# Optimization experiments

Measured on AMD Instinct MI355X. Metric: run time of the kernel, lower is better.

Reference implementation:

```python
import jax, jax.numpy as jnp
import numpy as np

N = 50000      # nodes
E = 500000     # edges
D_IN = 64      # node_in_dim
K = 4          # edge_in_dim
H = 64         # node_hidden_dim
C = 40         # num_class
L = 2          # num_layers


def setup_inputs() -> dict:
    key = jax.random.key(0)
    ks = jax.random.split(key, 10)
    node_features = jax.random.normal(ks[0], (N, D_IN), jnp.float32)
    edge_features = jax.random.normal(ks[1], (L, E, K), jnp.float32)
    src = jax.random.randint(ks[2], (E,), 0, N)
    dst = jax.random.randint(ks[3], (E,), 0, N)
    W0 = jax.random.normal(ks[4], (K * D_IN, H), jnp.float32) * 0.05
    b0 = jnp.zeros((H,), jnp.float32)
    W1 = jax.random.normal(ks[5], (K * H, H), jnp.float32) * 0.05
    b1 = jnp.zeros((H,), jnp.float32)
    Wfc = jax.random.normal(ks[6], (H, C), jnp.float32) * 0.05
    bfc = jnp.zeros((C,), jnp.float32)
    return dict(node_features=node_features, edge_features=edge_features,
                src=src, dst=dst, W0=W0, b0=b0, W1=W1, b1=b1, Wfc=Wfc, bfc=bfc)


def reference(node_features, edge_features, src, dst, W0, b0, W1, b1, Wfc, bfc):
    h = node_features  # [N, d]
    ones = jnp.ones((E,), jnp.float32)
    cnt = jnp.maximum(jax.ops.segment_sum(ones, dst, num_segments=N), 1.0)  # in-degree
    for i, (W, b) in enumerate([(W0, b0), (W1, b1)]):
        e = edge_features[i]          # [E, K]
        hs = h[src]                   # [E, d] edge gather of src node features
        d = hs.shape[1]
        # message: relu(Linear(flatten(e[:,:,None] * h[:,None,:])))
        # flatten order is (K, d), so reshape W -> [K, d, H] and contract directly
        Wr = W.reshape(K, d, H)
        m = jax.nn.relu(jnp.einsum('ek,ed,kdh->eh', e, hs, Wr) + b)  # [E, H]
        s = jax.ops.segment_sum(m, dst, num_segments=N)              # scatter-sum
        h = jax.nn.relu(s / cnt[:, None])                            # mailbox mean + relu
    return h @ Wfc + bfc  # [N, C]
```

## Files before the change

### kernel.cpp

```cpp
#include <hip/hip_runtime.h>
#include <hip/hip_fp16.h>

#define N_NODES 50000
#define N_EDGES 500000
#define DIM 64
#define KDIM 4
#define HID 64
#define NCLS 40
#define NBLK ((N_NODES + 255) / 256)

__device__ inline unsigned pack2(float a, float b) {
    __half2 h = __floats2half2_rn(a, b);
    return *(unsigned*)&h;
}
__device__ inline float2 unpack2(unsigned u) {
    __half2 h = *(__half2*)&u;
    return __half22float2(h);
}

__global__ void hist_k(const int* __restrict__ dst, int* __restrict__ cnt) {
    int e = blockIdx.x * 256 + threadIdx.x;
    if (e < N_EDGES) atomicAdd(&cnt[dst[e]], 1);
}

__global__ __launch_bounds__(256) void scan_k(const int* __restrict__ cnt,
                                              int* __restrict__ start,
                                              int* __restrict__ cursor,
                                              volatile int* __restrict__ bflag,
                                              volatile int* __restrict__ bval) {
    __shared__ int ls[256];
    __shared__ int sbase;
    __shared__ int ok_all;
    int b = blockIdx.x, t = threadIdx.x;
    int n = b * 256 + t;
    int v = (n < N_NODES) ? cnt[n] : 0;
    ls[t] = v;
    __syncthreads();
#pragma unroll
    for (int off = 1; off < 256; off <<= 1) {
        int u = (t >= off) ? ls[t - off] : 0;
        __syncthreads();
        ls[t] += u;
        __syncthreads();
    }
    int incl = ls[t];
    int total = ls[255];
    __syncthreads();

    if (t == 0) {
        bval[b] = total;
        __threadfence();
        bflag[b] = 1;
    }

    if (b > 0) {
        for (;;) {
            int f = (t < b) ? bflag[t] : 1;
            if (t == 0) ok_all = 1;
            __syncthreads();
            if (!f) ok_all = 0;
            __syncthreads();
            if (ok_all) break;
        }
        __threadfence();
        int pv = (t < b) ? bval[t] : 0;
        ls[t] = pv;
        __syncthreads();
#pragma unroll
        for (int off = 128; off > 0; off >>= 1) {
            if (t < off) ls[t] += ls[t + off];
            __syncthreads();
        }
        if (t == 0) sbase = ls[0];
        __syncthreads();
    } else {
        if (t == 0) sbase = 0;
        __syncthreads();
    }

    int excl = sbase + incl - v;
    if (n < N_NODES) { start[n] = excl; cursor[n] = excl; }
    if (n == 0) start[N_NODES] = N_EDGES;
}

__global__ void scatter_k(const int* __restrict__ src, const int* __restrict__ dst,
                          const float* __restrict__ ef, int* __restrict__ cursor,
                          uint4* __restrict__ rec) {
    int e = blockIdx.x * 256 + threadIdx.x;
    if (e < N_EDGES) {
        int d = dst[e];
        int pos = atomicAdd(&cursor[d], 1);
        int sn = src[e];
        float4 f0 = ((const float4*)ef)[e];
        float4 f1 = ((const float4*)ef)[N_EDGES + e];
        rec[2 * pos]     = make_uint4((unsigned)sn, pack2(f0.x, f0.y), pack2(f0.z, f0.w), 0u);
        rec[2 * pos + 1] = make_uint4((unsigned)sn, pack2(f1.x, f1.y), pack2(f1.z, f1.w), 0u);
    }
}

__global__ __launch_bounds__(256) void transform_k(const float* __restrict__ hin,
                                                   const float* __restrict__ W,
                                                   unsigned* __restrict__ y) {
    __shared__ float sW[2 * 64 * 64];
    __shared__ float sh[64 * 65];
    int t = threadIdx.x;
    int kpair = blockIdx.y;

    const float4* W4 = (const float4*)(W + (size_t)kpair * 2 * 4096);
    float4* sW4 = (float4*)sW;
#pragma unroll
    for (int i = 0; i < 8; ++i) sW4[t + 256 * i] = W4[t + 256 * i];

    int n0 = blockIdx.x * 64;
#pragma unroll
    for (int i = 0; i < 4; ++i) {
        int idx = t + 256 * i;
        int nl = idx >> 4;
        int dg = idx & 15;
        int n = n0 + nl;
        float4 v = make_float4(0.f, 0.f, 0.f, 0.f);
        if (n < N_NODES) v = ((const float4*)hin)[(size_t)n * 16 + dg];
        sh[nl * 65 + dg * 4 + 0] = v.x;
        sh[nl * 65 + dg * 4 + 1] = v.y;
        sh[nl * 65 + dg * 4 + 2] = v.z;
        sh[nl * 65 + dg * 4 + 3] = v.w;
    }
    __syncthreads();

    int nl = t & 31;
    int cg = t >> 5;
    int k_local = cg >> 2;
    int hc0 = (cg & 3) * 16;

    float acc0[16], acc1[16];
#pragma unroll
    for (int j = 0; j < 16; ++j) { acc0[j] = 0.f; acc1[j] = 0.f; }

    for (int d = 0; d < 64; ++d) {
        float a0 = sh[nl * 65 + d];
        float a1 = sh[(nl + 32) * 65 + d];
        const float* wr = &sW[k_local * 4096 + d * 64 + hc0];
#pragma unroll
        for (int j = 0; j < 16; ++j) {
            float w = wr[j];
            acc0[j] = fmaf(a0, w, acc0[j]);
            acc1[j] = fmaf(a1, w, acc1[j]);
        }
    }

    int n_a = n0 + nl, n_b = n0 + nl + 32;
    int cbase = (kpair * 2 + k_local) * 64 + hc0;
    if (n_a < N_NODES) {
        uint4* o = (uint4*)(y + ((size_t)n_a * 256 + cbase) / 2);
        o[0] = make_uint4(pack2(acc0[0], acc0[1]), pack2(acc0[2], acc0[3]),
                          pack2(acc0[4], acc0[5]), pack2(acc0[6], acc0[7]));
        o[1] = make_uint4(pack2(acc0[8], acc0[9]), pack2(acc0[10], acc0[11]),
                          pack2(acc0[12], acc0[13]), pack2(acc0[14], acc0[15]));
    }
    if (n_b < N_NODES) {
        uint4* o = (uint4*)(y + ((size_t)n_b * 256 + cbase) / 2);
        o[0] = make_uint4(pack2(acc1[0], acc1[1]), pack2(acc1[2], acc1[3]),
                          pack2(acc1[4], acc1[5]), pack2(acc1[6], acc1[7]));
        o[1] = make_uint4(pack2(acc1[8], acc1[9]), pack2(acc1[10], acc1[11]),
                          pack2(acc1[12], acc1[13]), pack2(acc1[14], acc1[15]));
    }
}

__device__ inline void load_edge(const uint4 r, const unsigned* __restrict__ y,
                                 int lane, uint2& q0, uint2& q1, uint2& q2, uint2& q3) {
    int sn = (int)r.x;
    const uint2* yb = (const uint2*)(y + (size_t)sn * 128);
    q0 = yb[lane];
    q1 = yb[16 + lane];
    q2 = yb[32 + lane];
    q3 = yb[48 + lane];
}

__device__ inline void compute_edge(const uint4 r, uint2 q0, uint2 q1, uint2 q2, uint2 q3,
                                    const float4 bias, float4& acc) {
    float2 e01 = unpack2(r.y);
    float2 e23 = unpack2(r.z);
    float2 a0 = unpack2(q0.x), a1 = unpack2(q0.y);
    float2 b0 = unpack2(q1.x), b1 = unpack2(q1.y);
    float2 c0 = unpack2(q2.x), c1 = unpack2(q2.y);
    float2 d0 = unpack2(q3.x), d1 = unpack2(q3.y);

    float4 z = bias;
    z.x = fmaf(e01.x, a0.x, z.x); z.y = fmaf(e01.x, a0.y, z.y);
    z.z = fmaf(e01.x, a1.x, z.z); z.w = fmaf(e01.x, a1.y, z.w);
    z.x = fmaf(e01.y, b0.x, z.x); z.y = fmaf(e01.y, b0.y, z.y);
    z.z = fmaf(e01.y, b1.x, z.z); z.w = fmaf(e01.y, b1.y, z.w);
    z.x = fmaf(e23.x, c0.x, z.x); z.y = fmaf(e23.x, c0.y, z.y);
    z.z = fmaf(e23.x, c1.x, z.z); z.w = fmaf(e23.x, c1.y, z.w);
    z.x = fmaf(e23.y, d0.x, z.x); z.y = fmaf(e23.y, d0.y, z.y);
    z.z = fmaf(e23.y, d1.x, z.z); z.w = fmaf(e23.y, d1.y, z.w);

    acc.x += fmaxf(z.x, 0.f);
    acc.y += fmaxf(z.y, 0.f);
    acc.z += fmaxf(z.z, 0.f);
    acc.w += fmaxf(z.w, 0.f);
}

__device__ inline float4 agg_core(const uint4* __restrict__ rec2,
                                  const int* __restrict__ start,
                                  const int* __restrict__ cnt,
                                  const unsigned* __restrict__ y,
                                  const float* __restrict__ b,
                                  int g, int lane) {
    int s0 = start[g];
    int deg = cnt[g];
    int s1 = s0 + deg;

    float4 bias = ((const float4*)b)[lane];
    float4 acc = make_float4(0.f, 0.f, 0.f, 0.f);

    int i = s0;
    for (; i + 4 <= s1; i += 4) {
        uint4 r0 = rec2[2 * i + 0];
        uint4 r1 = rec2[2 * i + 2];
        uint4 r2 = rec2[2 * i + 4];
        uint4 r3 = rec2[2 * i + 6];
        uint2 a0, a1, a2, a3, b0, b1, b2, b3, c0, c1, c2, c3, d0, d1, d2, d3;
        load_edge(r0, y, lane, a0, a1, a2, a3);
        load_edge(r1, y, lane, b0, b1, b2, b3);
        load_edge(r2, y, lane, c0, c1, c2, c3);
        load_edge(r3, y, lane, d0, d1, d2, d3);
        compute_edge(r0, a0, a1, a2, a3, bias, acc);
        compute_edge(r1, b0, b1, b2, b3, bias, acc);
        compute_edge(r2, c0, c1, c2, c3, bias, acc);
        compute_edge(r3, d0, d1, d2, d3, bias, acc);
    }
    if (i + 2 <= s1) {
        uint4 r0 = rec2[2 * i + 0];
        uint4 r1 = rec2[2 * i + 2];
        uint2 a0, a1, a2, a3, b0, b1, b2, b3;
        load_edge(r0, y, lane, a0, a1, a2, a3);
        load_edge(r1, y, lane, b0, b1, b2, b3);
        compute_edge(r0, a0, a1, a2, a3, bias, acc);
        compute_edge(r1, b0, b1, b2, b3, bias, acc);
        i += 2;
    }
    if (i < s1) {
        uint4 r0 = rec2[2 * i];
        uint2 a0, a1, a2, a3;
        load_edge(r0, y, lane, a0, a1, a2, a3);
        compute_edge(r0, a0, a1, a2, a3, bias, acc);
    }

    float inv = 1.0f / (float)(deg > 1 ? deg : 1);
    float4 r;
    r.x = fmaxf(acc.x * inv, 0.f);
    r.y = fmaxf(acc.y * inv, 0.f);
    r.z = fmaxf(acc.z * inv, 0.f);
    r.w = fmaxf(acc.w * inv, 0.f);
    return r;
}

__global__ __launch_bounds__(256) void agg_k(const uint4* __restrict__ rec2,
                                             const int* __restrict__ start,
                                             const int* __restrict__ cnt,
                                             const unsigned* __restrict__ y,
                                             const float* __restrict__ b,
                                             float* __restrict__ hout) {
    int t = blockIdx.x * 256 + threadIdx.x;
    int g = t >> 4;
    int lane = t & 15;
    float4 r = agg_core(rec2, start, cnt, y, b, g, lane);
    ((float4*)hout)[(size_t)g * 16 + lane] = r;
}

__global__ __launch_bounds__(256) void agg_fc_k(const uint4* __restrict__ rec2,
                                                const int* __restrict__ start,
                                                const int* __restrict__ cnt,
                                                const unsigned* __restrict__ y,
                                                const float* __restrict__ b,
                                                const float* __restrict__ Wfc,
                                                const float* __restrict__ bfc,
                                                float* __restrict__ out) {
    __shared__ float sh_h[16 * 65];
    __shared__ float sWfcT[NCLS * 65];
    __shared__ float sbfc[NCLS];
    int t = threadIdx.x;

    for (int i = t; i < 64 * NCLS; i += 256) {
        int j = i / NCLS;
        int c = i - j * NCLS;
        sWfcT[c * 65 + j] = Wfc[i];
    }
    if (t < NCLS) sbfc[t] = bfc[t];

    int nl = t >> 4;
    int lane = t & 15;
    int g = blockIdx.x * 16 + nl;

    float4 r = agg_core(rec2, start, cnt, y, b, g, lane);
    sh_h[nl * 65 + lane * 4 + 0] = r.x;
    sh_h[nl * 65 + lane * 4 + 1] = r.y;
    sh_h[nl * 65 + lane * 4 + 2] = r.z;
    sh_h[nl * 65 + lane * 4 + 3] = r.w;
    __syncthreads();

    for (int item = t; item < 16 * NCLS; item += 256) {
        int rn = item / NCLS;
        int c = item - rn * NCLS;
        float acc = sbfc[c];
        const float* hr = &sh_h[rn * 65];
        const float* wc = &sWfcT[c * 65];
#pragma unroll
        for (int j = 0; j < 64; ++j) acc = fmaf(hr[j], wc[j], acc);
        out[(size_t)(blockIdx.x * 16 + rn) * NCLS + c] = acc;
    }
}

extern "C" void kernel_launch(void* const* d_in, const int* in_sizes, int n_in,
                              void* d_out, int out_size, void* d_ws, size_t ws_size,
                              hipStream_t stream) {
    const float* nf  = (const float*)d_in[0];
    const float* ef  = (const float*)d_in[1];
    const int*   src = (const int*)d_in[2];
    const int*   dst = (const int*)d_in[3];
    const float* W0  = (const float*)d_in[4];
    const float* b0  = (const float*)d_in[5];
    const float* W1  = (const float*)d_in[6];
    const float* b1  = (const float*)d_in[7];
    const float* Wfc = (const float*)d_in[8];
    const float* bfc = (const float*)d_in[9];
    float* out = (float*)d_out;

    char* ws = (char*)d_ws;
    size_t off = 0;
    auto alloc = [&](size_t bytes) -> void* {
        void* p = ws + off;
        off = (off + bytes + 255) & ~(size_t)255;
        return p;
    };
    int*      zbuf   = (int*)     alloc((size_t)(50176 + 512) * 4);
    int*      cnt    = zbuf;
    int*      bflag  = zbuf + 50176;
    int*      bval   = zbuf + 50176 + 256;
    int*      start  = (int*)     alloc((size_t)(N_NODES + 1) * 4);
    int*      cursor = (int*)     alloc((size_t)N_NODES * 4);
    uint4*    rec    = (uint4*)   alloc((size_t)N_EDGES * 32);
    unsigned* y      = (unsigned*)alloc((size_t)N_NODES * 256 * 2);
    float*    hbuf   = (float*)   alloc((size_t)N_NODES * 64 * 4);

    hipMemsetAsync(zbuf, 0, (size_t)(50176 + 512) * 4, stream);

    hist_k<<<(N_EDGES + 255) / 256, 256, 0, stream>>>(dst, cnt);
    scan_k<<<NBLK, 256, 0, stream>>>(cnt, start, cursor, bflag, bval);
    scatter_k<<<(N_EDGES + 255) / 256, 256, 0, stream>>>(src, dst, ef, cursor, rec);

    dim3 tgrid((N_NODES + 63) / 64, 2);
    int agrid = N_NODES / 16;

    transform_k<<<tgrid, 256, 0, stream>>>(nf, W0, y);
    agg_k<<<agrid, 256, 0, stream>>>(rec, start, cnt, y, b0, hbuf);

    transform_k<<<tgrid, 256, 0, stream>>>(hbuf, W1, y);
    agg_fc_k<<<agrid, 256, 0, stream>>>(rec + 1, start, cnt, y, b1, Wfc, bfc, out);
}
```

Before: 300.1 us.

## Fuse all phases into one persistent cooperative kernel with grid syncs

```diff
diff --git a/kernel.cpp b/kernel.cpp
--- a/kernel.cpp
+++ b/kernel.cpp
@@ -1,5 +1,8 @@
 #include <hip/hip_runtime.h>
 #include <hip/hip_fp16.h>
+#include <hip/hip_cooperative_groups.h>
+
+namespace cg = cooperative_groups;
 
 #define N_NODES 50000
 #define N_EDGES 500000
@@ -8,6 +11,7 @@
 #define HID 64
 #define NCLS 40
 #define NBLK ((N_NODES + 255) / 256)
+#define ZN (50176 + 512)
 
 __device__ inline unsigned pack2(float a, float b) {
     __half2 h = __floats2half2_rn(a, b);
@@ -16,154 +20,6 @@
 __device__ inline float2 unpack2(unsigned u) {
     __half2 h = *(__half2*)&u;
     return __half22float2(h);
-}
-
-__global__ void hist_k(const int* __restrict__ dst, int* __restrict__ cnt) {
-    int e = blockIdx.x * 256 + threadIdx.x;
-    if (e < N_EDGES) atomicAdd(&cnt[dst[e]], 1);
-}
-
-__global__ __launch_bounds__(256) void scan_k(const int* __restrict__ cnt,
-                                              int* __restrict__ start,
-                                              int* __restrict__ cursor,
-                                              volatile int* __restrict__ bflag,
-                                              volatile int* __restrict__ bval) {
-    __shared__ int ls[256];
-    __shared__ int sbase;
-    __shared__ int ok_all;
-    int b = blockIdx.x, t = threadIdx.x;
-    int n = b * 256 + t;
-    int v = (n < N_NODES) ? cnt[n] : 0;
-    ls[t] = v;
-    __syncthreads();
-#pragma unroll
-    for (int off = 1; off < 256; off <<= 1) {
-        int u = (t >= off) ? ls[t - off] : 0;
-        __syncthreads();
-        ls[t] += u;
-        __syncthreads();
-    }
-    int incl = ls[t];
-    int total = ls[255];
-    __syncthreads();
-
-    if (t == 0) {
-        bval[b] = total;
-        __threadfence();
-        bflag[b] = 1;
-    }
-
-    if (b > 0) {
-        for (;;) {
-            int f = (t < b) ? bflag[t] : 1;
-            if (t == 0) ok_all = 1;
-            __syncthreads();
-            if (!f) ok_all = 0;
-            __syncthreads();
-            if (ok_all) break;
-        }
-        __threadfence();
-        int pv = (t < b) ? bval[t] : 0;
-        ls[t] = pv;
-        __syncthreads();
-#pragma unroll
-        for (int off = 128; off > 0; off >>= 1) {
-            if (t < off) ls[t] += ls[t + off];
-            __syncthreads();
-        }
-        if (t == 0) sbase = ls[0];
-        __syncthreads();
-    } else {
-        if (t == 0) sbase = 0;
-        __syncthreads();
-    }
-
-    int excl = sbase + incl - v;
-    if (n < N_NODES) { start[n] = excl; cursor[n] = excl; }
-    if (n == 0) start[N_NODES] = N_EDGES;
-}
-
-__global__ void scatter_k(const int* __restrict__ src, const int* __restrict__ dst,
-                          const float* __restrict__ ef, int* __restrict__ cursor,
-                          uint4* __restrict__ rec) {
-    int e = blockIdx.x * 256 + threadIdx.x;
-    if (e < N_EDGES) {
-        int d = dst[e];
-        int pos = atomicAdd(&cursor[d], 1);
-        int sn = src[e];
-        float4 f0 = ((const float4*)ef)[e];
-        float4 f1 = ((const float4*)ef)[N_EDGES + e];
-        rec[2 * pos]     = make_uint4((unsigned)sn, pack2(f0.x, f0.y), pack2(f0.z, f0.w), 0u);
-        rec[2 * pos + 1] = make_uint4((unsigned)sn, pack2(f1.x, f1.y), pack2(f1.z, f1.w), 0u);
-    }
-}
-
-__global__ __launch_bounds__(256) void transform_k(const float* __restrict__ hin,
-                                                   const float* __restrict__ W,
-                                                   unsigned* __restrict__ y) {
-    __shared__ float sW[2 * 64 * 64];
-    __shared__ float sh[64 * 65];
-    int t = threadIdx.x;
-    int kpair = blockIdx.y;
-
-    const float4* W4 = (const float4*)(W + (size_t)kpair * 2 * 4096);
-    float4* sW4 = (float4*)sW;
-#pragma unroll
-    for (int i = 0; i < 8; ++i) sW4[t + 256 * i] = W4[t + 256 * i];
-
-    int n0 = blockIdx.x * 64;
-#pragma unroll
-    for (int i = 0; i < 4; ++i) {
-        int idx = t + 256 * i;
-        int nl = idx >> 4;
-        int dg = idx & 15;
-        int n = n0 + nl;
-        float4 v = make_float4(0.f, 0.f, 0.f, 0.f);
-        if (n < N_NODES) v = ((const float4*)hin)[(size_t)n * 16 + dg];
-        sh[nl * 65 + dg * 4 + 0] = v.x;
-        sh[nl * 65 + dg * 4 + 1] = v.y;
-        sh[nl * 65 + dg * 4 + 2] = v.z;
-        sh[nl * 65 + dg * 4 + 3] = v.w;
-    }
-    __syncthreads();
-
-    int nl = t & 31;
-    int cg = t >> 5;
-    int k_local = cg >> 2;
-    int hc0 = (cg & 3) * 16;
-
-    float acc0[16], acc1[16];
-#pragma unroll
-    for (int j = 0; j < 16; ++j) { acc0[j] = 0.f; acc1[j] = 0.f; }
-
-    for (int d = 0; d < 64; ++d) {
-        float a0 = sh[nl * 65 + d];
-        float a1 = sh[(nl + 32) * 65 + d];
-        const float* wr = &sW[k_local * 4096 + d * 64 + hc0];
-#pragma unroll
-        for (int j = 0; j < 16; ++j) {
-            float w = wr[j];
-            acc0[j] = fmaf(a0, w, acc0[j]);
-            acc1[j] = fmaf(a1, w, acc1[j]);
-        }
-    }
-
-    int n_a = n0 + nl, n_b = n0 + nl + 32;
-    int cbase = (kpair * 2 + k_local) * 64 + hc0;
-    if (n_a < N_NODES) {
-        uint4* o = (uint4*)(y + ((size_t)n_a * 256 + cbase) / 2);
-        o[0] = make_uint4(pack2(acc0[0], acc0[1]), pack2(acc0[2], acc0[3]),
-                          pack2(acc0[4], acc0[5]), pack2(acc0[6], acc0[7]));
-        o[1] = make_uint4(pack2(acc0[8], acc0[9]), pack2(acc0[10], acc0[11]),
-                          pack2(acc0[12], acc0[13]), pack2(acc0[14], acc0[15]));
-    }
-    if (n_b < N_NODES) {
-        uint4* o = (uint4*)(y + ((size_t)n_b * 256 + cbase) / 2);
-        o[0] = make_uint4(pack2(acc1[0], acc1[1]), pack2(acc1[2], acc1[3]),
-                          pack2(acc1[4], acc1[5]), pack2(acc1[6], acc1[7]));
-        o[1] = make_uint4(pack2(acc1[8], acc1[9]), pack2(acc1[10], acc1[11]),
-                          pack2(acc1[12], acc1[13]), pack2(acc1[14], acc1[15]));
-    }
 }
 
 __device__ inline void load_edge(const uint4 r, const unsigned* __restrict__ y,
@@ -256,59 +112,203 @@
     return r;
 }
 
-__global__ __launch_bounds__(256) void agg_k(const uint4* __restrict__ rec2,
-                                             const int* __restrict__ start,
-                                             const int* __restrict__ cnt,
-                                             const unsigned* __restrict__ y,
-                                             const float* __restrict__ b,
-                                             float* __restrict__ hout) {
-    int t = blockIdx.x * 256 + threadIdx.x;
-    int g = t >> 4;
-    int lane = t & 15;
-    float4 r = agg_core(rec2, start, cnt, y, b, g, lane);
-    ((float4*)hout)[(size_t)g * 16 + lane] = r;
-}
-
-__global__ __launch_bounds__(256) void agg_fc_k(const uint4* __restrict__ rec2,
-                                                const int* __restrict__ start,
-                                                const int* __restrict__ cnt,
-                                                const unsigned* __restrict__ y,
-                                                const float* __restrict__ b,
-                                                const float* __restrict__ Wfc,
-                                                const float* __restrict__ bfc,
-                                                float* __restrict__ out) {
-    __shared__ float sh_h[16 * 65];
-    __shared__ float sWfcT[NCLS * 65];
-    __shared__ float sbfc[NCLS];
+__device__ inline void transform_phase(const float* __restrict__ hin,
+                                       const float* __restrict__ W,
+                                       unsigned* __restrict__ y,
+                                       float* smem, int t, int b, int gsz) {
+    float* sW = smem;
+    float* sh = smem + 4096;
+    const int NT = (N_NODES + 63) / 64;
+    for (int tile = b; tile < NT * 4; tile += gsz) {
+        int nt = tile >> 2;
+        int ks = tile & 3;
+        __syncthreads();
+        const float4* W4 = (const float4*)(W + (size_t)ks * 4096);
+        float4* sW4 = (float4*)sW;
+#pragma unroll
+        for (int i = 0; i < 4; ++i) sW4[t + 256 * i] = W4[t + 256 * i];
+        int n0 = nt * 64;
+#pragma unroll
+        for (int i = 0; i < 4; ++i) {
+            int idx = t + 256 * i;
+            int nl = idx >> 4;
+            int dg = idx & 15;
+            int n = n0 + nl;
+            float4 v = make_float4(0.f, 0.f, 0.f, 0.f);
+            if (n < N_NODES) v = ((const float4*)hin)[(size_t)n * 16 + dg];
+            sh[nl * 65 + dg * 4 + 0] = v.x;
+            sh[nl * 65 + dg * 4 + 1] = v.y;
+            sh[nl * 65 + dg * 4 + 2] = v.z;
+            sh[nl * 65 + dg * 4 + 3] = v.w;
+        }
+        __syncthreads();
+
+        int nl = t >> 2;
+        int cg = t & 3;
+        int hc0 = cg * 16;
+
+        float acc[16];
+#pragma unroll
+        for (int j = 0; j < 16; ++j) acc[j] = 0.f;
+
+        for (int d = 0; d < 64; ++d) {
+            float a0 = sh[nl * 65 + d];
+            const float* wr = &sW[d * 64 + hc0];
+#pragma unroll
+            for (int j = 0; j < 16; ++j) acc[j] = fmaf(a0, wr[j], acc[j]);
+        }
+
+        int n = n0 + nl;
+        if (n < N_NODES) {
+            uint4* o = (uint4*)(y + (size_t)n * 128 + ks * 32 + cg * 8);
+            o[0] = make_uint4(pack2(acc[0], acc[1]), pack2(acc[2], acc[3]),
+                              pack2(acc[4], acc[5]), pack2(acc[6], acc[7]));
+            o[1] = make_uint4(pack2(acc[8], acc[9]), pack2(acc[10], acc[11]),
+                              pack2(acc[12], acc[13]), pack2(acc[14], acc[15]));
+        }
+    }
+}
+
+__global__ __launch_bounds__(256, 4) void fused_k(
+    const float* __restrict__ nf, const float* __restrict__ ef,
+    const int* __restrict__ src, const int* __restrict__ dst,
+    const float* __restrict__ W0, const float* __restrict__ b0,
+    const float* __restrict__ W1, const float* __restrict__ b1,
+    const float* __restrict__ Wfc, const float* __restrict__ bfc,
+    float* __restrict__ out,
+    int* cnt, int* bflag, int* bval, int* start, int* cursor,
+    uint4* rec, unsigned* y, float* hbuf) {
+    cg::grid_group grid = cg::this_grid();
+    __shared__ float smem[8256];
     int t = threadIdx.x;
-
-    for (int i = t; i < 64 * NCLS; i += 256) {
-        int j = i / NCLS;
-        int c = i - j * NCLS;
-        sWfcT[c * 65 + j] = Wfc[i];
-    }
-    if (t < NCLS) sbfc[t] = bfc[t];
-
-    int nl = t >> 4;
-    int lane = t & 15;
-    int g = blockIdx.x * 16 + nl;
-
-    float4 r = agg_core(rec2, start, cnt, y, b, g, lane);
-    sh_h[nl * 65 + lane * 4 + 0] = r.x;
-    sh_h[nl * 65 + lane * 4 + 1] = r.y;
-    sh_h[nl * 65 + lane * 4 + 2] = r.z;
-    sh_h[nl * 65 + lane * 4 + 3] = r.w;
-    __syncthreads();
-
-    for (int item = t; item < 16 * NCLS; item += 256) {
-        int rn = item / NCLS;
-        int c = item - rn * NCLS;
-        float acc = sbfc[c];
-        const float* hr = &sh_h[rn * 65];
-        const float* wc = &sWfcT[c * 65];
-#pragma unroll
-        for (int j = 0; j < 64; ++j) acc = fmaf(hr[j], wc[j], acc);
-        out[(size_t)(blockIdx.x * 16 + rn) * NCLS + c] = acc;
+    int b = blockIdx.x;
+    int gsz = gridDim.x;
+    int gtid = b * 256 + t;
+    int gthreads = gsz * 256;
+
+    for (int i = gtid; i < ZN; i += gthreads) cnt[i] = 0;
+    grid.sync();
+
+    for (int e = gtid; e < N_EDGES; e += gthreads) atomicAdd(&cnt[dst[e]], 1);
+    grid.sync();
+
+    if (b < NBLK) {
+        int* ls = (int*)smem;
+        int n = b * 256 + t;
+        int v = (n < N_NODES) ? cnt[n] : 0;
+        ls[t] = v;
+        __syncthreads();
+#pragma unroll
+        for (int off = 1; off < 256; off <<= 1) {
+            int u = (t >= off) ? ls[t - off] : 0;
+            __syncthreads();
+            ls[t] += u;
+            __syncthreads();
+        }
+        int incl = ls[t];
+        int total = ls[255];
+        __syncthreads();
+
+        if (t == 0) {
+            bval[b] = total;
+            __threadfence();
+            bflag[b] = 1;
+        }
+
+        if (b > 0) {
+            volatile int* vf = (volatile int*)bflag;
+            for (;;) {
+                int f = (t < b) ? vf[t] : 1;
+                if (t == 0) ls[256] = 1;
+                __syncthreads();
+                if (!f) ls[256] = 0;
+                __syncthreads();
+                if (ls[256]) break;
+            }
+            __threadfence();
+            int pv = (t < b) ? bval[t] : 0;
+            ls[t] = pv;
+            __syncthreads();
+#pragma unroll
+            for (int off = 128; off > 0; off >>= 1) {
+                if (t < off) ls[t] += ls[t + off];
+                __syncthreads();
+            }
+            if (t == 0) ls[257] = ls[0];
+            __syncthreads();
+        } else {
+            if (t == 0) ls[257] = 0;
+            __syncthreads();
+        }
+
+        int excl = ls[257] + incl - v;
+        if (n < N_NODES) { start[n] = excl; cursor[n] = excl; }
+        if (n == 0) start[N_NODES] = N_EDGES;
+    }
+    grid.sync();
+
+    for (int e = gtid; e < N_EDGES; e += gthreads) {
+        int d = dst[e];
+        int pos = atomicAdd(&cursor[d], 1);
+        int sn = src[e];
+        float4 f0 = ((const float4*)ef)[e];
+        float4 f1 = ((const float4*)ef)[N_EDGES + e];
+        rec[2 * pos]     = make_uint4((unsigned)sn, pack2(f0.x, f0.y), pack2(f0.z, f0.w), 0u);
+        rec[2 * pos + 1] = make_uint4((unsigned)sn, pack2(f1.x, f1.y), pack2(f1.z, f1.w), 0u);
+    }
+    grid.sync();
+
+    transform_phase(nf, W0, y, smem, t, b, gsz);
+    grid.sync();
+
+    {
+        int nl = t >> 4;
+        int lane = t & 15;
+        for (int nb = b; nb < N_NODES / 16; nb += gsz) {
+            int g = nb * 16 + nl;
+            float4 r = agg_core(rec, start, cnt, y, b0, g, lane);
+            ((float4*)hbuf)[(size_t)g * 16 + lane] = r;
+        }
+    }
+    grid.sync();
+
+    transform_phase(hbuf, W1, y, smem, t, b, gsz);
+    grid.sync();
+
+    {
+        float* sh_h  = smem;
+        float* sWfcT = smem + 16 * 65;
+        float* sbfc  = smem + 16 * 65 + NCLS * 65;
+        for (int i = t; i < 64 * NCLS; i += 256) {
+            int j = i / NCLS;
+            int c = i - j * NCLS;
+            sWfcT[c * 65 + j] = Wfc[i];
+        }
+        if (t < NCLS) sbfc[t] = bfc[t];
+        __syncthreads();
+
+        int nl = t >> 4;
+        int lane = t & 15;
+        for (int nb = b; nb < N_NODES / 16; nb += gsz) {
+            int g = nb * 16 + nl;
+            float4 r = agg_core(rec + 1, start, cnt, y, b1, g, lane);
+            sh_h[nl * 65 + lane * 4 + 0] = r.x;
+            sh_h[nl * 65 + lane * 4 + 1] = r.y;
+            sh_h[nl * 65 + lane * 4 + 2] = r.z;
+            sh_h[nl * 65 + lane * 4 + 3] = r.w;
+            __syncthreads();
+            for (int item = t; item < 16 * NCLS; item += 256) {
+                int rn = item / NCLS;
+                int c = item - rn * NCLS;
+                float acc = sbfc[c];
+                const float* hr = &sh_h[rn * 65];
+                const float* wc = &sWfcT[c * 65];
+#pragma unroll
+                for (int j = 0; j < 64; ++j) acc = fmaf(hr[j], wc[j], acc);
+                out[(size_t)(nb * 16 + rn) * NCLS + c] = acc;
+            }
+            __syncthreads();
+        }
     }
 }
 
@@ -334,7 +334,7 @@
         off = (off + bytes + 255) & ~(size_t)255;
         return p;
     };
-    int*      zbuf   = (int*)     alloc((size_t)(50176 + 512) * 4);
+    int*      zbuf   = (int*)     alloc((size_t)ZN * 4);
     int*      cnt    = zbuf;
     int*      bflag  = zbuf + 50176;
     int*      bval   = zbuf + 50176 + 256;
@@ -344,18 +344,17 @@
     unsigned* y      = (unsigned*)alloc((size_t)N_NODES * 256 * 2);
     float*    hbuf   = (float*)   alloc((size_t)N_NODES * 64 * 4);
 
-    hipMemsetAsync(zbuf, 0, (size_t)(50176 + 512) * 4, stream);
-
-    hist_k<<<(N_EDGES + 255) / 256, 256, 0, stream>>>(dst, cnt);
-    scan_k<<<NBLK, 256, 0, stream>>>(cnt, start, cursor, bflag, bval);
-    scatter_k<<<(N_EDGES + 255) / 256, 256, 0, stream>>>(src, dst, ef, cursor, rec);
-
-    dim3 tgrid((N_NODES + 63) / 64, 2);
-    int agrid = N_NODES / 16;
-
-    transform_k<<<tgrid, 256, 0, stream>>>(nf, W0, y);
-    agg_k<<<agrid, 256, 0, stream>>>(rec, start, cnt, y, b0, hbuf);
-
-    transform_k<<<tgrid, 256, 0, stream>>>(hbuf, W1, y);
-    agg_fc_k<<<agrid, 256, 0, stream>>>(rec + 1, start, cnt, y, b1, Wfc, bfc, out);
-}
+    int occ = 0;
+    if (hipOccupancyMaxActiveBlocksPerMultiprocessor(&occ, fused_k, 256, 0) != hipSuccess || occ < 1)
+        occ = 1;
+    int grid = occ * 256;
+    if (grid > 1024) grid = 1024;
+    if (grid < 256) grid = 256;
+
+    void* args[] = { (void*)&nf, (void*)&ef, (void*)&src, (void*)&dst,
+                     (void*)&W0, (void*)&b0, (void*)&W1, (void*)&b1,
+                     (void*)&Wfc, (void*)&bfc, (void*)&out,
+                     (void*)&cnt, (void*)&bflag, (void*)&bval, (void*)&start,
+                     (void*)&cursor, (void*)&rec, (void*)&y, (void*)&hbuf };
+    hipLaunchCooperativeKernel((const void*)fused_k, dim3(grid), dim3(256), args, 0, stream);
+}
```

Measured after the change: 784.2 us. 161% more time.

## Fuse pipeline into three persistent kernels with grid barriers and fp16 weights

Applied to the files above, without the earlier changes.

```diff
diff --git a/kernel.cpp b/kernel.cpp
--- a/kernel.cpp
+++ b/kernel.cpp
@@ -8,6 +8,9 @@
 #define HID 64
 #define NCLS 40
 #define NBLK ((N_NODES + 255) / 256)
+#define NGRP (N_NODES / 16)
+#define NUNITS (782 * 2)
+#define ZN (50176 + 8 + 256 + 256)
 
 __device__ inline unsigned pack2(float a, float b) {
     __half2 h = __floats2half2_rn(a, b);
@@ -18,100 +21,37 @@
     return __half22float2(h);
 }
 
-__global__ void hist_k(const int* __restrict__ dst, int* __restrict__ cnt) {
-    int e = blockIdx.x * 256 + threadIdx.x;
-    if (e < N_EDGES) atomicAdd(&cnt[dst[e]], 1);
-}
-
-__global__ __launch_bounds__(256) void scan_k(const int* __restrict__ cnt,
-                                              int* __restrict__ start,
-                                              int* __restrict__ cursor,
-                                              volatile int* __restrict__ bflag,
-                                              volatile int* __restrict__ bval) {
-    __shared__ int ls[256];
-    __shared__ int sbase;
-    __shared__ int ok_all;
-    int b = blockIdx.x, t = threadIdx.x;
-    int n = b * 256 + t;
-    int v = (n < N_NODES) ? cnt[n] : 0;
-    ls[t] = v;
-    __syncthreads();
-#pragma unroll
-    for (int off = 1; off < 256; off <<= 1) {
-        int u = (t >= off) ? ls[t - off] : 0;
-        __syncthreads();
-        ls[t] += u;
-        __syncthreads();
-    }
-    int incl = ls[t];
-    int total = ls[255];
-    __syncthreads();
-
+__device__ inline void gbar(int* bar, int t) {
+    __syncthreads();
     if (t == 0) {
-        bval[b] = total;
         __threadfence();
-        bflag[b] = 1;
-    }
-
-    if (b > 0) {
-        for (;;) {
-            int f = (t < b) ? bflag[t] : 1;
-            if (t == 0) ok_all = 1;
-            __syncthreads();
-            if (!f) ok_all = 0;
-            __syncthreads();
-            if (ok_all) break;
+        atomicAdd(bar, 1);
+        while (__hip_atomic_load(bar, __ATOMIC_RELAXED, __HIP_MEMORY_SCOPE_AGENT)
+               < (int)gridDim.x) {
+            __builtin_amdgcn_s_sleep(8);
         }
         __threadfence();
-        int pv = (t < b) ? bval[t] : 0;
-        ls[t] = pv;
-        __syncthreads();
-#pragma unroll
-        for (int off = 128; off > 0; off >>= 1) {
-            if (t < off) ls[t] += ls[t + off];
-            __syncthreads();
-        }
-        if (t == 0) sbase = ls[0];
-        __syncthreads();
-    } else {
-        if (t == 0) sbase = 0;
-        __syncthreads();
-    }
-
-    int excl = sbase + incl - v;
-    if (n < N_NODES) { start[n] = excl; cursor[n] = excl; }
-    if (n == 0) start[N_NODES] = N_EDGES;
-}
-
-__global__ void scatter_k(const int* __restrict__ src, const int* __restrict__ dst,
-                          const float* __restrict__ ef, int* __restrict__ cursor,
-                          uint4* __restrict__ rec) {
-    int e = blockIdx.x * 256 + threadIdx.x;
-    if (e < N_EDGES) {
-        int d = dst[e];
-        int pos = atomicAdd(&cursor[d], 1);
-        int sn = src[e];
-        float4 f0 = ((const float4*)ef)[e];
-        float4 f1 = ((const float4*)ef)[N_EDGES + e];
-        rec[2 * pos]     = make_uint4((unsigned)sn, pack2(f0.x, f0.y), pack2(f0.z, f0.w), 0u);
-        rec[2 * pos + 1] = make_uint4((unsigned)sn, pack2(f1.x, f1.y), pack2(f1.z, f1.w), 0u);
-    }
-}
-
-__global__ __launch_bounds__(256) void transform_k(const float* __restrict__ hin,
-                                                   const float* __restrict__ W,
-                                                   unsigned* __restrict__ y) {
-    __shared__ float sW[2 * 64 * 64];
-    __shared__ float sh[64 * 65];
-    int t = threadIdx.x;
-    int kpair = blockIdx.y;
-
-    const float4* W4 = (const float4*)(W + (size_t)kpair * 2 * 4096);
-    float4* sW4 = (float4*)sW;
-#pragma unroll
-    for (int i = 0; i < 8; ++i) sW4[t + 256 * i] = W4[t + 256 * i];
-
-    int n0 = blockIdx.x * 64;
+    }
+    __syncthreads();
+}
+
+__device__ inline void transform_unit(const float* __restrict__ hin,
+                                      const float* __restrict__ W,
+                                      unsigned* __restrict__ y,
+                                      int u, int t, __half* sW, float* sh) {
+    int nt = u >> 1;
+    int kp = u & 1;
+    __syncthreads();
+    const float4* W4 = (const float4*)(W + (size_t)kp * 8192);
+    __half2* sW2 = (__half2*)sW;
+#pragma unroll
+    for (int i = 0; i < 8; ++i) {
+        int idx = t + 256 * i;
+        float4 v = W4[idx];
+        sW2[2 * idx]     = __floats2half2_rn(v.x, v.y);
+        sW2[2 * idx + 1] = __floats2half2_rn(v.z, v.w);
+    }
+    int n0 = nt * 64;
 #pragma unroll
     for (int i = 0; i < 4; ++i) {
         int idx = t + 256 * i;
@@ -129,7 +69,7 @@
 
     int nl = t & 31;
     int cg = t >> 5;
-    int k_local = cg >> 2;
+    int kl = cg >> 2;
     int hc0 = (cg & 3) * 16;
 
     float acc0[16], acc1[16];
@@ -139,17 +79,19 @@
     for (int d = 0; d < 64; ++d) {
         float a0 = sh[nl * 65 + d];
         float a1 = sh[(nl + 32) * 65 + d];
-        const float* wr = &sW[k_local * 4096 + d * 64 + hc0];
-#pragma unroll
-        for (int j = 0; j < 16; ++j) {
-            float w = wr[j];
-            acc0[j] = fmaf(a0, w, acc0[j]);
-            acc1[j] = fmaf(a1, w, acc1[j]);
+        const __half2* wr = (const __half2*)(sW + kl * 4096 + d * 64 + hc0);
+#pragma unroll
+        for (int j = 0; j < 8; ++j) {
+            float2 w2 = __half22float2(wr[j]);
+            acc0[2 * j]     = fmaf(a0, w2.x, acc0[2 * j]);
+            acc0[2 * j + 1] = fmaf(a0, w2.y, acc0[2 * j + 1]);
+            acc1[2 * j]     = fmaf(a1, w2.x, acc1[2 * j]);
+            acc1[2 * j + 1] = fmaf(a1, w2.y, acc1[2 * j + 1]);
         }
     }
 
     int n_a = n0 + nl, n_b = n0 + nl + 32;
-    int cbase = (kpair * 2 + k_local) * 64 + hc0;
+    int cbase = (kp * 2 + kl) * 64 + hc0;
     if (n_a < N_NODES) {
         uint4* o = (uint4*)(y + ((size_t)n_a * 256 + cbase) / 2);
         o[0] = make_uint4(pack2(acc0[0], acc0[1]), pack2(acc0[2], acc0[3]),
@@ -256,59 +198,171 @@
     return r;
 }
 
-__global__ __launch_bounds__(256) void agg_k(const uint4* __restrict__ rec2,
-                                             const int* __restrict__ start,
-                                             const int* __restrict__ cnt,
-                                             const unsigned* __restrict__ y,
-                                             const float* __restrict__ b,
-                                             float* __restrict__ hout) {
-    int t = blockIdx.x * 256 + threadIdx.x;
-    int g = t >> 4;
-    int lane = t & 15;
-    float4 r = agg_core(rec2, start, cnt, y, b, g, lane);
-    ((float4*)hout)[(size_t)g * 16 + lane] = r;
-}
-
-__global__ __launch_bounds__(256) void agg_fc_k(const uint4* __restrict__ rec2,
-                                                const int* __restrict__ start,
-                                                const int* __restrict__ cnt,
-                                                const unsigned* __restrict__ y,
-                                                const float* __restrict__ b,
-                                                const float* __restrict__ Wfc,
-                                                const float* __restrict__ bfc,
-                                                float* __restrict__ out) {
-    __shared__ float sh_h[16 * 65];
-    __shared__ float sWfcT[NCLS * 65];
-    __shared__ float sbfc[NCLS];
+__global__ __launch_bounds__(256, 4) void front_k(const float* __restrict__ nf,
+                                                  const float* __restrict__ W0,
+                                                  unsigned* __restrict__ y,
+                                                  const int* __restrict__ dst,
+                                                  int* __restrict__ cnt) {
+    __shared__ __align__(16) char smem[33024];
+    __half* sW = (__half*)smem;
+    float* sh = (float*)(smem + 16384);
     int t = threadIdx.x;
 
-    for (int i = t; i < 64 * NCLS; i += 256) {
-        int j = i / NCLS;
-        int c = i - j * NCLS;
-        sWfcT[c * 65 + j] = Wfc[i];
-    }
-    if (t < NCLS) sbfc[t] = bfc[t];
-
-    int nl = t >> 4;
-    int lane = t & 15;
-    int g = blockIdx.x * 16 + nl;
-
-    float4 r = agg_core(rec2, start, cnt, y, b, g, lane);
-    sh_h[nl * 65 + lane * 4 + 0] = r.x;
-    sh_h[nl * 65 + lane * 4 + 1] = r.y;
-    sh_h[nl * 65 + lane * 4 + 2] = r.z;
-    sh_h[nl * 65 + lane * 4 + 3] = r.w;
-    __syncthreads();
-
-    for (int item = t; item < 16 * NCLS; item += 256) {
-        int rn = item / NCLS;
-        int c = item - rn * NCLS;
-        float acc = sbfc[c];
-        const float* hr = &sh_h[rn * 65];
-        const float* wc = &sWfcT[c * 65];
-#pragma unroll
-        for (int j = 0; j < 64; ++j) acc = fmaf(hr[j], wc[j], acc);
-        out[(size_t)(blockIdx.x * 16 + rn) * NCLS + c] = acc;
+    for (int u = blockIdx.x; u < NUNITS; u += gridDim.x)
+        transform_unit(nf, W0, y, u, t, sW, sh);
+
+    int gtid = blockIdx.x * 256 + t;
+    int gth = gridDim.x * 256;
+    for (int e = gtid; e < N_EDGES; e += gth) atomicAdd(&cnt[dst[e]], 1);
+}
+
+__global__ __launch_bounds__(256) void mid_k(const int* __restrict__ cnt,
+                                             int* __restrict__ start,
+                                             int* __restrict__ cursor,
+                                             volatile int* __restrict__ bflag,
+                                             volatile int* __restrict__ bval,
+                                             int* __restrict__ bar0,
+                                             const int* __restrict__ src,
+                                             const int* __restrict__ dst,
+                                             const float* __restrict__ ef,
+                                             uint4* __restrict__ rec) {
+    __shared__ int ls[258];
+    int b = blockIdx.x, t = threadIdx.x;
+    int n = b * 256 + t;
+    int v = (n < N_NODES) ? cnt[n] : 0;
+    ls[t] = v;
+    __syncthreads();
+#pragma unroll
+    for (int off = 1; off < 256; off <<= 1) {
+        int u = (t >= off) ? ls[t - off] : 0;
+        __syncthreads();
+        ls[t] += u;
+        __syncthreads();
+    }
+    int incl = ls[t];
+    int total = ls[255];
+    __syncthreads();
+
+    if (t == 0) {
+        ((int*)bval)[b] = total;
+        __threadfence();
+        ((int*)bflag)[b] = 1;
+    }
+
+    if (b > 0) {
+        for (;;) {
+            int f = (t < b) ? bflag[t] : 1;
+            if (t == 0) ls[256] = 1;
+            __syncthreads();
+            if (!f) ls[256] = 0;
+            __syncthreads();
+            if (ls[256]) break;
+        }
+        __threadfence();
+        int pv = (t < b) ? bval[t] : 0;
+        ls[t] = pv;
+        __syncthreads();
+#pragma unroll
+        for (int off = 128; off > 0; off >>= 1) {
+            if (t < off) ls[t] += ls[t + off];
+            __syncthreads();
+        }
+        if (t == 0) ls[257] = ls[0];
+        __syncthreads();
+    } else {
+        if (t == 0) ls[257] = 0;
+        __syncthreads();
+    }
+
+    int excl = ls[257] + incl - v;
+    if (n < N_NODES) { start[n] = excl; cursor[n] = excl; }
+    if (n == 0) start[N_NODES] = N_EDGES;
+
+    gbar(bar0, t);
+
+    int gtid = b * 256 + t;
+    int gth = gridDim.x * 256;
+    for (int e = gtid; e < N_EDGES; e += gth) {
+        int d = dst[e];
+        int pos = atomicAdd(&cursor[d], 1);
+        int sn = src[e];
+        float4 f0 = ((const float4*)ef)[e];
+        float4 f1 = ((const float4*)ef)[N_EDGES + e];
+        rec[2 * pos]     = make_uint4((unsigned)sn, pack2(f0.x, f0.y), pack2(f0.z, f0.w), 0u);
+        rec[2 * pos + 1] = make_uint4((unsigned)sn, pack2(f1.x, f1.y), pack2(f1.z, f1.w), 0u);
+    }
+}
+
+__global__ __launch_bounds__(256, 4) void back_k(const uint4* __restrict__ rec,
+                                                 const int* __restrict__ start,
+                                                 const int* __restrict__ cnt,
+                                                 unsigned* __restrict__ y,
+                                                 const float* __restrict__ b0,
+                                                 const float* __restrict__ W1,
+                                                 const float* __restrict__ b1,
+                                                 const float* __restrict__ Wfc,
+                                                 const float* __restrict__ bfc,
+                                                 float* __restrict__ hbuf,
+                                                 float* __restrict__ out,
+                                                 int* __restrict__ bar1,
+                                                 int* __restrict__ bar2) {
+    __shared__ __align__(16) char smem[33024];
+    int t = threadIdx.x;
+
+    {
+        int nl = t >> 4;
+        int lane = t & 15;
+        for (int nb = blockIdx.x; nb < NGRP; nb += gridDim.x) {
+            int g = nb * 16 + nl;
+            float4 r = agg_core(rec, start, cnt, y, b0, g, lane);
+            ((float4*)hbuf)[(size_t)g * 16 + lane] = r;
+        }
+    }
+    gbar(bar1, t);
+
+    {
+        __half* sW = (__half*)smem;
+        float* sh = (float*)(smem + 16384);
+        for (int u = blockIdx.x; u < NUNITS; u += gridDim.x)
+            transform_unit(hbuf, W1, y, u, t, sW, sh);
+    }
+    gbar(bar2, t);
+
+    {
+        float* sh_h  = (float*)smem;
+        float* sWfcT = (float*)(smem + 4160);
+        float* sbfc  = (float*)(smem + 4160 + 10400);
+        __syncthreads();
+        for (int i = t; i < 64 * NCLS; i += 256) {
+            int j = i / NCLS;
+            int c = i - j * NCLS;
+            sWfcT[c * 65 + j] = Wfc[i];
+        }
+        if (t < NCLS) sbfc[t] = bfc[t];
+        __syncthreads();
+
+        int nl = t >> 4;
+        int lane = t & 15;
+        for (int nb = blockIdx.x; nb < NGRP; nb += gridDim.x) {
+            int g = nb * 16 + nl;
+            float4 r = agg_core(rec + 1, start, cnt, y, b1, g, lane);
+            sh_h[nl * 65 + lane * 4 + 0] = r.x;
+            sh_h[nl * 65 + lane * 4 + 1] = r.y;
+            sh_h[nl * 65 + lane * 4 + 2] = r.z;
+            sh_h[nl * 65 + lane * 4 + 3] = r.w;
+            __syncthreads();
+            for (int item = t; item < 16 * NCLS; item += 256) {
+                int rn = item / NCLS;
+                int c = item - rn * NCLS;
+                float acc = sbfc[c];
+                const float* hr = &sh_h[rn * 65];
+                const float* wc = &sWfcT[c * 65];
+#pragma unroll
+                for (int j = 0; j < 64; ++j) acc = fmaf(hr[j], wc[j], acc);
+                out[(size_t)(nb * 16 + rn) * NCLS + c] = acc;
+            }
+            __syncthreads();
+        }
     }
 }
 
@@ -334,28 +388,28 @@
         off = (off + bytes + 255) & ~(size_t)255;
         return p;
     };
-    int*      zbuf   = (int*)     alloc((size_t)(50176 + 512) * 4);
+    int*      zbuf   = (int*)     alloc((size_t)ZN * 4);
     int*      cnt    = zbuf;
-    int*      bflag  = zbuf + 50176;
-    int*      bval   = zbuf + 50176 + 256;
+    int*      bar    = zbuf + 50176;
+    int*      bflag  = zbuf + 50176 + 8;
+    int*      bval   = zbuf + 50176 + 8 + 256;
     int*      start  = (int*)     alloc((size_t)(N_NODES + 1) * 4);
     int*      cursor = (int*)     alloc((size_t)N_NODES * 4);
     uint4*    rec    = (uint4*)   alloc((size_t)N_EDGES * 32);
     unsigned* y      = (unsigned*)alloc((size_t)N_NODES * 256 * 2);
     float*    hbuf   = (float*)   alloc((size_t)N_NODES * 64 * 4);
 
-    hipMemsetAsync(zbuf, 0, (size_t)(50176 + 512) * 4, stream);
-
-    hist_k<<<(N_EDGES + 255) / 256, 256, 0, stream>>>(dst, cnt);
-    scan_k<<<NBLK, 256, 0, stream>>>(cnt, start, cursor, bflag, bval);
-    scatter_k<<<(N_EDGES + 255) / 256, 256, 0, stream>>>(src, dst, ef, cursor, rec);
-
-    dim3 tgrid((N_NODES + 63) / 64, 2);
-    int agrid = N_NODES / 16;
-
-    transform_k<<<tgrid, 256, 0, stream>>>(nf, W0, y);
-    agg_k<<<agrid, 256, 0, stream>>>(rec, start, cnt, y, b0, hbuf);
-
-    transform_k<<<tgrid, 256, 0, stream>>>(hbuf, W1, y);
-    agg_fc_k<<<agrid, 256, 0, stream>>>(rec + 1, start, cnt, y, b1, Wfc, bfc, out);
-}
+    hipMemsetAsync(zbuf, 0, (size_t)ZN * 4, stream);
+
+    front_k<<<1024, 256, 0, stream>>>(nf, W0, y, dst, cnt);
+    mid_k<<<NBLK, 256, 0, stream>>>(cnt, start, cursor, bflag, bval, bar + 0,
+                                    src, dst, ef, rec);
+
+    int occ = 0;
+    if (hipOccupancyMaxActiveBlocksPerMultiprocessor(&occ, back_k, 256, 0) != hipSuccess || occ < 1)
+        occ = 1;
+    if (occ > 4) occ = 4;
+    int gridC = occ * 256;
+    back_k<<<gridC, 256, 0, stream>>>(rec, start, cnt, y, b0, W1, b1, Wfc, bfc,
+                                      hbuf, out, bar + 1, bar + 2);
+}
```

Result: slower. 459.7 us (+53.2%).
